# Kernel optimization log

Hardware: AMD Instinct MI355X
Metric: run time of the kernel (lower is better)

## Reference

```python
import jax, jax.numpy as jnp
import numpy as np

T, B, I, H, O = 512, 128, 512, 1024, 256

def setup_inputs() -> dict:
    key = jax.random.key(0)
    ks = jax.random.split(key, 7)
    s = 1.0 / np.sqrt(H)
    return {
        "seqs": jax.random.normal(ks[0], (T, B, I), dtype=jnp.float32),
        "W_ih": jax.random.uniform(ks[1], (H, I), minval=-s, maxval=s, dtype=jnp.float32),
        "W_hh": jax.random.uniform(ks[2], (H, H), minval=-s, maxval=s, dtype=jnp.float32),
        "b_ih": jax.random.uniform(ks[3], (H,), minval=-s, maxval=s, dtype=jnp.float32),
        "b_hh": jax.random.uniform(ks[4], (H,), minval=-s, maxval=s, dtype=jnp.float32),
        "W_fc": jax.random.uniform(ks[5], (O, H), minval=-s, maxval=s, dtype=jnp.float32),
        "b_fc": jax.random.uniform(ks[6], (O,), minval=-s, maxval=s, dtype=jnp.float32),
    }

def reference(seqs, W_ih, W_hh, b_ih, b_hh, W_fc, b_fc):
    # Precompute input projections for all timesteps in one big GEMM: [T,B,H]
    x_proj = jnp.einsum('tbi,hi->tbh', seqs, W_ih) + b_ih + b_hh

    def step(h, xp):
        h_new = jax.nn.relu(xp + h @ W_hh.T)
        return h_new, None

    h0 = jnp.zeros((seqs.shape[1], W_hh.shape[0]), dtype=seqs.dtype)
    h_final, _ = jax.lax.scan(step, h0, x_proj)
    return h_final @ W_fc.T + b_fc
```

## Files before the change

### kernel.cpp

```cpp
#include <hip/hip_runtime.h>
#include <hip/hip_bf16.h>
#include <stdint.h>

#define T_STEPS 512
#define BATCH   128
#define IN      512
#define HID     1024
#define OUTN    256

typedef __bf16 bf16x8 __attribute__((ext_vector_type(8)));
typedef float  f32x4  __attribute__((ext_vector_type(4)));
typedef unsigned short us8 __attribute__((ext_vector_type(8)));
typedef unsigned int   ui4 __attribute__((ext_vector_type(4)));

__device__ __forceinline__ unsigned short f2bf(float f) {
    uint32_t u = __float_as_uint(f);
    uint32_t r = (u + 0x7fffu + ((u >> 16) & 1u)) >> 16;
    return (unsigned short)r;
}

__device__ __forceinline__ ui4 ld_u128_agent(const void* p) {
    ui4 v;
    asm volatile("global_load_dwordx4 %0, %1, off sc0 sc1"
                 : "=v"(v) : "v"(p) : "memory");
    return v;
}

__device__ __forceinline__ bf16x8 ld_frag(const unsigned short* smem, int row, int kbyte, int rowstride) {
    int off = row * rowstride + (kbyte ^ ((row & 7) << 4));
    return *reinterpret_cast<const bf16x8*>(reinterpret_cast<const char*>(smem) + off);
}

__global__ __launch_bounds__(256, 1) void rnn_persistent(
    const float* __restrict__ seqs, const float* __restrict__ W_ih,
    const float* __restrict__ W_hh, const float* __restrict__ b_ih,
    const float* __restrict__ b_hh, const float* __restrict__ W_fc,
    const float* __restrict__ b_fc, float* __restrict__ out,
    unsigned short* __restrict__ hbuf,
    float* __restrict__ hfinal,
    unsigned int* __restrict__ flags)
{
    const int tid  = threadIdx.x;
    const int lane = tid & 63;
    const int wv   = tid >> 6;
    const int wg   = blockIdx.x;
    const int g    = wg >> 5;
    const int w    = wg & 31;
    const int gr0  = g * 16;
    const int c0   = w * 32;
    const int ln15 = lane & 15;
    const int lk   = lane >> 4;

    __shared__ unsigned short xtile[16 * 512];
    __shared__ unsigned short htile[16 * 1024];
    __shared__ float red[4][16][33];
    __shared__ float biasS[32];

    bf16x8 wih[2][4];
    bf16x8 whh[2][8];
    #pragma unroll
    for (int nt = 0; nt < 2; nt++) {
        const int j = c0 + nt * 16 + ln15;
        #pragma unroll
        for (int s = 0; s < 4; s++) {
            const int k = wv * 128 + s * 32 + lk * 8;
            const float* p = W_ih + j * IN + k;
            us8 u;
            #pragma unroll
            for (int e = 0; e < 8; e++) u[e] = f2bf(p[e]);
            wih[nt][s] = __builtin_bit_cast(bf16x8, u);
        }
        #pragma unroll
        for (int s = 0; s < 8; s++) {
            const int k = wv * 256 + s * 32 + lk * 8;
            const float* p = W_hh + j * HID + k;
            us8 u;
            #pragma unroll
            for (int e = 0; e < 8; e++) u[e] = f2bf(p[e]);
            whh[nt][s] = __builtin_bit_cast(bf16x8, u);
        }
    }
    if (tid < 32) biasS[tid] = b_ih[c0 + tid] + b_hh[c0 + tid];

    unsigned int* grp_flags = flags + g * 32;
    unsigned int* my_flag   = grp_flags + w;

    const int xrow[4] = { (tid) >> 6, (tid + 256) >> 6, (tid + 512) >> 6, (tid + 768) >> 6 };
    const int xcol[4] = { (tid) & 63, (tid + 256) & 63, (tid + 512) & 63, (tid + 768) & 63 };

    us8 xbf[4];
    {
        const float* xsrc = seqs + (size_t)gr0 * IN;
        #pragma unroll
        for (int it = 0; it < 4; it++) {
            const float* s4 = xsrc + xrow[it] * IN + xcol[it] * 8;
            float4 a = *reinterpret_cast<const float4*>(s4);
            float4 b = *reinterpret_cast<const float4*>(s4 + 4);
            us8 u;
            u[0]=f2bf(a.x); u[1]=f2bf(a.y); u[2]=f2bf(a.z); u[3]=f2bf(a.w);
            u[4]=f2bf(b.x); u[5]=f2bf(b.y); u[6]=f2bf(b.z); u[7]=f2bf(b.w);
            xbf[it] = u;
        }
    }

    for (int t = 0; t < T_STEPS; t++) {
        #pragma unroll
        for (int it = 0; it < 4; it++) {
            const int off = xrow[it] * 1024 + ((xcol[it] * 16) ^ ((xrow[it] & 7) << 4));
            *reinterpret_cast<us8*>(reinterpret_cast<char*>(xtile) + off) = xbf[it];
        }

        if (t > 0 && wv == 0 && lane < 32) {
            const unsigned int* f = grp_flags + lane;
            while (__hip_atomic_load(f, __ATOMIC_RELAXED, __HIP_MEMORY_SCOPE_AGENT) < (unsigned)t) {
                __builtin_amdgcn_s_sleep(1);
            }
        }
        __syncthreads();

        ui4 hv[8];
        if (t > 0) {
            const char* hsrc = reinterpret_cast<const char*>(
                hbuf + (size_t)(t & 1) * (BATCH * HID) + (size_t)gr0 * HID);
            #pragma unroll
            for (int it = 0; it < 8; it++) {
                const int c    = tid + it * 256;
                const int row  = c >> 7;
                const int colc = c & 127;
                hv[it] = ld_u128_agent(hsrc + row * 2048 + colc * 16);
            }
        }

        float4 xr[8];
        {
            const int tn = (t + 1 < T_STEPS) ? t + 1 : t;
            const float* xsrc = seqs + (size_t)tn * (BATCH * IN) + (size_t)gr0 * IN;
            #pragma unroll
            for (int it = 0; it < 4; it++) {
                const float* s4 = xsrc + xrow[it] * IN + xcol[it] * 8;
                xr[2*it]   = *reinterpret_cast<const float4*>(s4);
                xr[2*it+1] = *reinterpret_cast<const float4*>(s4 + 4);
            }
        }

        f32x4 acc0 = {0.f, 0.f, 0.f, 0.f};
        f32x4 acc1 = {0.f, 0.f, 0.f, 0.f};
        {
            const int kx0b = wv * 256;
            #pragma unroll
            for (int s = 0; s < 4; s++) {
                bf16x8 a = ld_frag(xtile, ln15, kx0b + s * 64 + lk * 16, 1024);
                acc0 = __builtin_amdgcn_mfma_f32_16x16x32_bf16(a, wih[0][s], acc0, 0, 0, 0);
                acc1 = __builtin_amdgcn_mfma_f32_16x16x32_bf16(a, wih[1][s], acc1, 0, 0, 0);
            }
        }

        if (t > 0) {
            asm volatile("s_waitcnt vmcnt(8)" ::: "memory");
            __builtin_amdgcn_sched_barrier(0);
            #pragma unroll
            for (int it = 0; it < 8; it++) {
                const int c    = tid + it * 256;
                const int row  = c >> 7;
                const int colc = c & 127;
                const int off = row * 2048 + ((colc * 16) ^ ((row & 7) << 4));
                *reinterpret_cast<ui4*>(reinterpret_cast<char*>(htile) + off) = hv[it];
            }
            __syncthreads();

            const int kh0b = wv * 512;
            #pragma unroll
            for (int s = 0; s < 8; s++) {
                bf16x8 a = ld_frag(htile, ln15, kh0b + s * 64 + lk * 16, 2048);
                acc0 = __builtin_amdgcn_mfma_f32_16x16x32_bf16(a, whh[0][s], acc0, 0, 0, 0);
                acc1 = __builtin_amdgcn_mfma_f32_16x16x32_bf16(a, whh[1][s], acc1, 0, 0, 0);
            }
        }

        #pragma unroll
        for (int r = 0; r < 4; r++) {
            red[wv][lk * 4 + r][ln15]      = acc0[r];
            red[wv][lk * 4 + r][16 + ln15] = acc1[r];
        }
        __syncthreads();
        {
            const int row = tid >> 4;
            const int co2 = (tid & 15) * 2;
            float v0 = red[0][row][co2]   + red[1][row][co2]   + red[2][row][co2]   + red[3][row][co2]   + biasS[co2];
            float v1 = red[0][row][co2+1] + red[1][row][co2+1] + red[2][row][co2+1] + red[3][row][co2+1] + biasS[co2+1];
            v0 = fmaxf(v0, 0.0f);
            v1 = fmaxf(v1, 0.0f);

            asm volatile("s_waitcnt vmcnt(0)" ::: "memory");
            __builtin_amdgcn_sched_barrier(0);
            #pragma unroll
            for (int it = 0; it < 4; it++) {
                float4 a = xr[2*it], b = xr[2*it+1];
                us8 u;
                u[0]=f2bf(a.x); u[1]=f2bf(a.y); u[2]=f2bf(a.z); u[3]=f2bf(a.w);
                u[4]=f2bf(b.x); u[5]=f2bf(b.y); u[6]=f2bf(b.z); u[7]=f2bf(b.w);
                xbf[it] = u;
            }

            if (t < T_STEPS - 1) {
                unsigned pack = (unsigned)f2bf(v0) | ((unsigned)f2bf(v1) << 16);
                unsigned* dst = reinterpret_cast<unsigned*>(
                    hbuf + (size_t)((t + 1) & 1) * (BATCH * HID) + (size_t)(gr0 + row) * HID + c0 + co2);
                __hip_atomic_store(dst, pack, __ATOMIC_RELAXED, __HIP_MEMORY_SCOPE_AGENT);
            } else {
                unsigned long long pack = ((unsigned long long)__float_as_uint(v1) << 32) | __float_as_uint(v0);
                unsigned long long* dst = reinterpret_cast<unsigned long long*>(
                    hfinal + (size_t)(gr0 + row) * HID + c0 + co2);
                __hip_atomic_store(dst, pack, __ATOMIC_RELAXED, __HIP_MEMORY_SCOPE_AGENT);
            }
        }
        asm volatile("s_waitcnt vmcnt(0)" ::: "memory");
        __syncthreads();
        if (tid == 0) {
            __hip_atomic_store(my_flag, (unsigned)(t + 1), __ATOMIC_RELAXED, __HIP_MEMORY_SCOPE_AGENT);
        }
    }

    if (wv == 0 && lane < 32) {
        const unsigned int* f = grp_flags + lane;
        while (__hip_atomic_load(f, __ATOMIC_RELAXED, __HIP_MEMORY_SCOPE_AGENT) < (unsigned)T_STEPS) {
            __builtin_amdgcn_s_sleep(1);
        }
    }
    __syncthreads();
    __threadfence();

    {
        const int oi   = tid & 127;
        const int half = tid >> 7;
        const int brow = gr0 + (oi >> 3);
        const int o    = w * 8 + (oi & 7);
        const float* hv2 = hfinal + (size_t)brow * HID + half * 512;
        const float* wf  = W_fc  + (size_t)o * HID + half * 512;
        float sum = 0.f;
        #pragma unroll 4
        for (int k = 0; k < 512; k += 4) {
            float4 hh = *reinterpret_cast<const float4*>(hv2 + k);
            float4 ww = *reinterpret_cast<const float4*>(wf + k);
            sum += hh.x * ww.x + hh.y * ww.y + hh.z * ww.z + hh.w * ww.w;
        }
        float* redf = &red[0][0][0];
        redf[tid] = sum;
        __syncthreads();
        if (tid < 128) {
            out[(size_t)brow * OUTN + o] = redf[tid] + redf[tid + 128] + b_fc[o];
        }
    }
}

extern "C" void kernel_launch(void* const* d_in, const int* in_sizes, int n_in,
                              void* d_out, int out_size, void* d_ws, size_t ws_size,
                              hipStream_t stream) {
    const float* seqs = (const float*)d_in[0];
    const float* W_ih = (const float*)d_in[1];
    const float* W_hh = (const float*)d_in[2];
    const float* b_ih = (const float*)d_in[3];
    const float* b_hh = (const float*)d_in[4];
    const float* W_fc = (const float*)d_in[5];
    const float* b_fc = (const float*)d_in[6];
    float* out = (float*)d_out;

    char* ws = (char*)d_ws;
    unsigned short* hbuf   = (unsigned short*)ws;
    float*          hfinal = (float*)(ws + 524288);
    unsigned int*   flags  = (unsigned int*)(ws + 1048576);

    hipMemsetAsync(flags, 0, 1024, stream);
    rnn_persistent<<<dim3(256), dim3(256), 0, stream>>>(
        seqs, W_ih, W_hh, b_ih, b_hh, W_fc, b_fc, out, hbuf, hfinal, flags);
}
```

Measured before the change: 1.396 ms.

## Replace per-step flag barrier with parity-tagged hidden-state data polling

```diff
diff --git a/kernel.cpp b/kernel.cpp
--- a/kernel.cpp
+++ b/kernel.cpp
@@ -13,6 +13,9 @@
 typedef unsigned short us8 __attribute__((ext_vector_type(8)));
 typedef unsigned int   ui4 __attribute__((ext_vector_type(4)));
 
+#define TAGM 0x80008000u
+#define CLRM 0x7FFF7FFFu
+
 __device__ __forceinline__ unsigned short f2bf(float f) {
     uint32_t u = __float_as_uint(f);
     uint32_t r = (u + 0x7fffu + ((u >> 16) & 1u)) >> 16;
@@ -30,15 +33,17 @@
     int off = row * rowstride + (kbyte ^ ((row & 7) << 4));
     return *reinterpret_cast<const bf16x8*>(reinterpret_cast<const char*>(smem) + off);
 }
+__device__ __forceinline__ us8 ld_frag_u(const unsigned short* smem, int row, int kbyte, int rowstride) {
+    int off = row * rowstride + (kbyte ^ ((row & 7) << 4));
+    return *reinterpret_cast<const us8*>(reinterpret_cast<const char*>(smem) + off);
+}
 
 __global__ __launch_bounds__(256, 1) void rnn_persistent(
     const float* __restrict__ seqs, const float* __restrict__ W_ih,
     const float* __restrict__ W_hh, const float* __restrict__ b_ih,
     const float* __restrict__ b_hh, const float* __restrict__ W_fc,
     const float* __restrict__ b_fc, float* __restrict__ out,
-    unsigned short* __restrict__ hbuf,
-    float* __restrict__ hfinal,
-    unsigned int* __restrict__ flags)
+    unsigned short* __restrict__ hbuf)
 {
     const int tid  = threadIdx.x;
     const int lane = tid & 63;
@@ -82,8 +87,15 @@
     }
     if (tid < 32) biasS[tid] = b_ih[c0 + tid] + b_hh[c0 + tid];
 
-    unsigned int* grp_flags = flags + g * 32;
-    unsigned int* my_flag   = grp_flags + w;
+    int hgoff[8], hloff[8];
+    #pragma unroll
+    for (int it = 0; it < 8; it++) {
+        const int c    = tid + it * 256;
+        const int row  = c >> 7;
+        const int colc = c & 127;
+        hgoff[it] = row * 2048 + colc * 16;
+        hloff[it] = row * 2048 + ((colc * 16) ^ ((row & 7) << 4));
+    }
 
     const int xrow[4] = { (tid) >> 6, (tid + 256) >> 6, (tid + 512) >> 6, (tid + 768) >> 6 };
     const int xcol[4] = { (tid) & 63, (tid + 256) & 63, (tid + 512) & 63, (tid + 768) & 63 };
@@ -103,33 +115,24 @@
         }
     }
 
+    const size_t slotB = (size_t)BATCH * HID * 2;
+    char* hbase = reinterpret_cast<char*>(hbuf);
+
     for (int t = 0; t < T_STEPS; t++) {
         #pragma unroll
         for (int it = 0; it < 4; it++) {
             const int off = xrow[it] * 1024 + ((xcol[it] * 16) ^ ((xrow[it] & 7) << 4));
             *reinterpret_cast<us8*>(reinterpret_cast<char*>(xtile) + off) = xbf[it];
         }
-
-        if (t > 0 && wv == 0 && lane < 32) {
-            const unsigned int* f = grp_flags + lane;
-            while (__hip_atomic_load(f, __ATOMIC_RELAXED, __HIP_MEMORY_SCOPE_AGENT) < (unsigned)t) {
-                __builtin_amdgcn_s_sleep(1);
-            }
-        }
         __syncthreads();
 
         ui4 hv[8];
+        const char* hsrc = hbase + (size_t)(t & 1) * slotB + (size_t)gr0 * HID * 2;
         if (t > 0) {
-            const char* hsrc = reinterpret_cast<const char*>(
-                hbuf + (size_t)(t & 1) * (BATCH * HID) + (size_t)gr0 * HID);
-            #pragma unroll
-            for (int it = 0; it < 8; it++) {
-                const int c    = tid + it * 256;
-                const int row  = c >> 7;
-                const int colc = c & 127;
-                hv[it] = ld_u128_agent(hsrc + row * 2048 + colc * 16);
-            }
-        }
+            #pragma unroll
+            for (int it = 0; it < 8; it++) hv[it] = ld_u128_agent(hsrc + hgoff[it]);
+        }
+        __builtin_amdgcn_sched_barrier(0);
 
         float4 xr[8];
         {
@@ -142,6 +145,7 @@
                 xr[2*it+1] = *reinterpret_cast<const float4*>(s4 + 4);
             }
         }
+        __builtin_amdgcn_sched_barrier(0);
 
         f32x4 acc0 = {0.f, 0.f, 0.f, 0.f};
         f32x4 acc1 = {0.f, 0.f, 0.f, 0.f};
@@ -156,15 +160,33 @@
         }
 
         if (t > 0) {
+            const unsigned pr = ((t >> 1) & 1) ? 0x80000000u : 0x00008000u;
             asm volatile("s_waitcnt vmcnt(8)" ::: "memory");
             __builtin_amdgcn_sched_barrier(0);
+            unsigned pending = 0xFFu;
+            while (true) {
+                unsigned np = 0;
+                #pragma unroll
+                for (int it = 0; it < 8; it++) {
+                    if (pending & (1u << it)) {
+                        unsigned d = ((hv[it][0] & TAGM) ^ pr) | ((hv[it][1] & TAGM) ^ pr)
+                                   | ((hv[it][2] & TAGM) ^ pr) | ((hv[it][3] & TAGM) ^ pr);
+                        if (d != 0u) {
+                            np |= (1u << it);
+                            hv[it] = ld_u128_agent(hsrc + hgoff[it]);
+                        }
+                    }
+                }
+                pending = np;
+                if (pending == 0u) break;
+                asm volatile("s_waitcnt vmcnt(0)" ::: "memory");
+                __builtin_amdgcn_sched_barrier(0);
+            }
             #pragma unroll
             for (int it = 0; it < 8; it++) {
-                const int c    = tid + it * 256;
-                const int row  = c >> 7;
-                const int colc = c & 127;
-                const int off = row * 2048 + ((colc * 16) ^ ((row & 7) << 4));
-                *reinterpret_cast<ui4*>(reinterpret_cast<char*>(htile) + off) = hv[it];
+                ui4 v = hv[it];
+                v[0] &= CLRM; v[1] &= CLRM; v[2] &= CLRM; v[3] &= CLRM;
+                *reinterpret_cast<ui4*>(reinterpret_cast<char*>(htile) + hloff[it]) = v;
             }
             __syncthreads();
 
@@ -183,72 +205,92 @@
             red[wv][lk * 4 + r][16 + ln15] = acc1[r];
         }
         __syncthreads();
+        const int hrow = tid >> 4;
+        const int co2  = (tid & 15) * 2;
+        float v0 = red[0][hrow][co2]   + red[1][hrow][co2]   + red[2][hrow][co2]   + red[3][hrow][co2]   + biasS[co2];
+        float v1 = red[0][hrow][co2+1] + red[1][hrow][co2+1] + red[2][hrow][co2+1] + red[3][hrow][co2+1] + biasS[co2+1];
+        v0 = fmaxf(v0, 0.0f);
+        v1 = fmaxf(v1, 0.0f);
+
+        asm volatile("s_waitcnt vmcnt(0)" ::: "memory");
+        __builtin_amdgcn_sched_barrier(0);
+        #pragma unroll
+        for (int it = 0; it < 4; it++) {
+            float4 a = xr[2*it], b = xr[2*it+1];
+            us8 u;
+            u[0]=f2bf(a.x); u[1]=f2bf(a.y); u[2]=f2bf(a.z); u[3]=f2bf(a.w);
+            u[4]=f2bf(b.x); u[5]=f2bf(b.y); u[6]=f2bf(b.z); u[7]=f2bf(b.w);
+            xbf[it] = u;
+        }
+
         {
-            const int row = tid >> 4;
-            const int co2 = (tid & 15) * 2;
-            float v0 = red[0][row][co2]   + red[1][row][co2]   + red[2][row][co2]   + red[3][row][co2]   + biasS[co2];
-            float v1 = red[0][row][co2+1] + red[1][row][co2+1] + red[2][row][co2+1] + red[3][row][co2+1] + biasS[co2+1];
-            v0 = fmaxf(v0, 0.0f);
-            v1 = fmaxf(v1, 0.0f);
-
+            const unsigned pw = (((t + 1) >> 1) & 1) ? 0x80000000u : 0x00008000u;
+            unsigned pack = (unsigned)f2bf(v0) | ((unsigned)f2bf(v1) << 16) | pw;
+            unsigned* dst = reinterpret_cast<unsigned*>(
+                hbase + (size_t)((t + 1) & 1) * slotB
+                + ((size_t)(gr0 + hrow) * HID + c0 + co2) * 2);
+            __hip_atomic_store(dst, pack, __ATOMIC_RELAXED, __HIP_MEMORY_SCOPE_AGENT);
+        }
+    }
+
+    {
+        const char* hsrc = hbase + (size_t)gr0 * HID * 2;
+        ui4 hv[8];
+        #pragma unroll
+        for (int it = 0; it < 8; it++) hv[it] = ld_u128_agent(hsrc + hgoff[it]);
+        unsigned pending = 0xFFu;
+        do {
             asm volatile("s_waitcnt vmcnt(0)" ::: "memory");
             __builtin_amdgcn_sched_barrier(0);
-            #pragma unroll
-            for (int it = 0; it < 4; it++) {
-                float4 a = xr[2*it], b = xr[2*it+1];
-                us8 u;
-                u[0]=f2bf(a.x); u[1]=f2bf(a.y); u[2]=f2bf(a.z); u[3]=f2bf(a.w);
-                u[4]=f2bf(b.x); u[5]=f2bf(b.y); u[6]=f2bf(b.z); u[7]=f2bf(b.w);
-                xbf[it] = u;
-            }
-
-            if (t < T_STEPS - 1) {
-                unsigned pack = (unsigned)f2bf(v0) | ((unsigned)f2bf(v1) << 16);
-                unsigned* dst = reinterpret_cast<unsigned*>(
-                    hbuf + (size_t)((t + 1) & 1) * (BATCH * HID) + (size_t)(gr0 + row) * HID + c0 + co2);
-                __hip_atomic_store(dst, pack, __ATOMIC_RELAXED, __HIP_MEMORY_SCOPE_AGENT);
-            } else {
-                unsigned long long pack = ((unsigned long long)__float_as_uint(v1) << 32) | __float_as_uint(v0);
-                unsigned long long* dst = reinterpret_cast<unsigned long long*>(
-                    hfinal + (size_t)(gr0 + row) * HID + c0 + co2);
-                __hip_atomic_store(dst, pack, __ATOMIC_RELAXED, __HIP_MEMORY_SCOPE_AGENT);
-            }
-        }
-        asm volatile("s_waitcnt vmcnt(0)" ::: "memory");
+            unsigned np = 0;
+            #pragma unroll
+            for (int it = 0; it < 8; it++) {
+                if (pending & (1u << it)) {
+                    unsigned d = ((hv[it][0] & TAGM) ^ 0x00008000u) | ((hv[it][1] & TAGM) ^ 0x00008000u)
+                               | ((hv[it][2] & TAGM) ^ 0x00008000u) | ((hv[it][3] & TAGM) ^ 0x00008000u);
+                    if (d != 0u) {
+                        np |= (1u << it);
+                        hv[it] = ld_u128_agent(hsrc + hgoff[it]);
+                    }
+                }
+            }
+            pending = np;
+        } while (pending);
+        #pragma unroll
+        for (int it = 0; it < 8; it++) {
+            ui4 v = hv[it];
+            v[0] &= CLRM; v[1] &= CLRM; v[2] &= CLRM; v[3] &= CLRM;
+            *reinterpret_cast<ui4*>(reinterpret_cast<char*>(htile) + hloff[it]) = v;
+        }
         __syncthreads();
-        if (tid == 0) {
-            __hip_atomic_store(my_flag, (unsigned)(t + 1), __ATOMIC_RELAXED, __HIP_MEMORY_SCOPE_AGENT);
-        }
-    }
-
-    if (wv == 0 && lane < 32) {
-        const unsigned int* f = grp_flags + lane;
-        while (__hip_atomic_load(f, __ATOMIC_RELAXED, __HIP_MEMORY_SCOPE_AGENT) < (unsigned)T_STEPS) {
-            __builtin_amdgcn_s_sleep(1);
-        }
-    }
-    __syncthreads();
-    __threadfence();
+    }
 
     {
         const int oi   = tid & 127;
         const int half = tid >> 7;
-        const int brow = gr0 + (oi >> 3);
+        const int row  = oi >> 3;
         const int o    = w * 8 + (oi & 7);
-        const float* hv2 = hfinal + (size_t)brow * HID + half * 512;
-        const float* wf  = W_fc  + (size_t)o * HID + half * 512;
+        const float* wf = W_fc + (size_t)o * HID + half * 512;
         float sum = 0.f;
         #pragma unroll 4
-        for (int k = 0; k < 512; k += 4) {
-            float4 hh = *reinterpret_cast<const float4*>(hv2 + k);
-            float4 ww = *reinterpret_cast<const float4*>(wf + k);
-            sum += hh.x * ww.x + hh.y * ww.y + hh.z * ww.z + hh.w * ww.w;
+        for (int ck = 0; ck < 64; ck++) {
+            us8 hu = ld_frag_u(htile, row, half * 1024 + ck * 16, 2048);
+            float4 wa = *reinterpret_cast<const float4*>(wf + ck * 8);
+            float4 wb = *reinterpret_cast<const float4*>(wf + ck * 8 + 4);
+            sum += __uint_as_float((unsigned)hu[0] << 16) * wa.x
+                 + __uint_as_float((unsigned)hu[1] << 16) * wa.y
+                 + __uint_as_float((unsigned)hu[2] << 16) * wa.z
+                 + __uint_as_float((unsigned)hu[3] << 16) * wa.w
+                 + __uint_as_float((unsigned)hu[4] << 16) * wb.x
+                 + __uint_as_float((unsigned)hu[5] << 16) * wb.y
+                 + __uint_as_float((unsigned)hu[6] << 16) * wb.z
+                 + __uint_as_float((unsigned)hu[7] << 16) * wb.w;
         }
         float* redf = &red[0][0][0];
         redf[tid] = sum;
         __syncthreads();
         if (tid < 128) {
-            out[(size_t)brow * OUTN + o] = redf[tid] + redf[tid + 128] + b_fc[o];
+            out[(size_t)(gr0 + row) * OUTN + o] = redf[tid] + redf[tid + 128] + b_fc[o];
         }
     }
 }
@@ -265,12 +307,9 @@
     const float* b_fc = (const float*)d_in[6];
     float* out = (float*)d_out;
 
-    char* ws = (char*)d_ws;
-    unsigned short* hbuf   = (unsigned short*)ws;
-    float*          hfinal = (float*)(ws + 524288);
-    unsigned int*   flags  = (unsigned int*)(ws + 1048576);
-
-    hipMemsetAsync(flags, 0, 1024, stream);
+    unsigned short* hbuf = (unsigned short*)d_ws;
+
+    hipMemsetAsync(hbuf, 0, 2 * BATCH * HID * sizeof(unsigned short), stream);
     rnn_persistent<<<dim3(256), dim3(256), 0, stream>>>(
-        seqs, W_ih, W_hh, b_ih, b_hh, W_fc, b_fc, out, hbuf, hfinal, flags);
-}
+        seqs, W_ih, W_hh, b_ih, b_hh, W_fc, b_fc, out, hbuf);
+}
```

Result: slower. 1.594 ms (+14.2%).

## Load recurrent h fragments straight into MFMA registers and pad flags

Applied to the files above, without the earlier changes.

```diff
diff --git a/kernel.cpp b/kernel.cpp
--- a/kernel.cpp
+++ b/kernel.cpp
@@ -52,7 +52,6 @@
     const int lk   = lane >> 4;
 
     __shared__ unsigned short xtile[16 * 512];
-    __shared__ unsigned short htile[16 * 1024];
     __shared__ float red[4][16][33];
     __shared__ float biasS[32];
 
@@ -82,8 +81,10 @@
     }
     if (tid < 32) biasS[tid] = b_ih[c0 + tid] + b_hh[c0 + tid];
 
-    unsigned int* grp_flags = flags + g * 32;
-    unsigned int* my_flag   = grp_flags + w;
+    unsigned int* grp_flags = flags + g * 32 * 16;
+    unsigned int* my_flag   = grp_flags + w * 16;
+
+    const int hfrag = ln15 * 2048 + wv * 512 + lk * 16;
 
     const int xrow[4] = { (tid) >> 6, (tid + 256) >> 6, (tid + 512) >> 6, (tid + 768) >> 6 };
     const int xcol[4] = { (tid) & 63, (tid + 256) & 63, (tid + 512) & 63, (tid + 768) & 63 };
@@ -103,32 +104,14 @@
         }
     }
 
+    const size_t slotB = (size_t)BATCH * HID * 2;
+    char* hbase = reinterpret_cast<char*>(hbuf);
+
     for (int t = 0; t < T_STEPS; t++) {
         #pragma unroll
         for (int it = 0; it < 4; it++) {
             const int off = xrow[it] * 1024 + ((xcol[it] * 16) ^ ((xrow[it] & 7) << 4));
             *reinterpret_cast<us8*>(reinterpret_cast<char*>(xtile) + off) = xbf[it];
-        }
-
-        if (t > 0 && wv == 0 && lane < 32) {
-            const unsigned int* f = grp_flags + lane;
-            while (__hip_atomic_load(f, __ATOMIC_RELAXED, __HIP_MEMORY_SCOPE_AGENT) < (unsigned)t) {
-                __builtin_amdgcn_s_sleep(1);
-            }
-        }
-        __syncthreads();
-
-        ui4 hv[8];
-        if (t > 0) {
-            const char* hsrc = reinterpret_cast<const char*>(
-                hbuf + (size_t)(t & 1) * (BATCH * HID) + (size_t)gr0 * HID);
-            #pragma unroll
-            for (int it = 0; it < 8; it++) {
-                const int c    = tid + it * 256;
-                const int row  = c >> 7;
-                const int colc = c & 127;
-                hv[it] = ld_u128_agent(hsrc + row * 2048 + colc * 16);
-            }
         }
 
         float4 xr[8];
@@ -143,6 +126,22 @@
             }
         }
 
+        if (t > 0 && wv == 0 && lane < 32) {
+            const unsigned int* f = grp_flags + lane * 16;
+            while (__hip_atomic_load(f, __ATOMIC_RELAXED, __HIP_MEMORY_SCOPE_AGENT) < (unsigned)t) {
+                __builtin_amdgcn_s_sleep(1);
+            }
+        }
+        __syncthreads();
+
+        ui4 hv[8];
+        if (t > 0) {
+            const char* hsrc = hbase + (size_t)(t & 1) * slotB + (size_t)gr0 * 2048 + hfrag;
+            #pragma unroll
+            for (int s = 0; s < 8; s++) hv[s] = ld_u128_agent(hsrc + s * 64);
+        }
+        __builtin_amdgcn_sched_barrier(0);
+
         f32x4 acc0 = {0.f, 0.f, 0.f, 0.f};
         f32x4 acc1 = {0.f, 0.f, 0.f, 0.f};
         {
@@ -156,22 +155,11 @@
         }
 
         if (t > 0) {
-            asm volatile("s_waitcnt vmcnt(8)" ::: "memory");
+            asm volatile("s_waitcnt vmcnt(0)" ::: "memory");
             __builtin_amdgcn_sched_barrier(0);
             #pragma unroll
-            for (int it = 0; it < 8; it++) {
-                const int c    = tid + it * 256;
-                const int row  = c >> 7;
-                const int colc = c & 127;
-                const int off = row * 2048 + ((colc * 16) ^ ((row & 7) << 4));
-                *reinterpret_cast<ui4*>(reinterpret_cast<char*>(htile) + off) = hv[it];
-            }
-            __syncthreads();
-
-            const int kh0b = wv * 512;
-            #pragma unroll
             for (int s = 0; s < 8; s++) {
-                bf16x8 a = ld_frag(htile, ln15, kh0b + s * 64 + lk * 16, 2048);
+                bf16x8 a = __builtin_bit_cast(bf16x8, hv[s]);
                 acc0 = __builtin_amdgcn_mfma_f32_16x16x32_bf16(a, whh[0][s], acc0, 0, 0, 0);
                 acc1 = __builtin_amdgcn_mfma_f32_16x16x32_bf16(a, whh[1][s], acc1, 0, 0, 0);
             }
@@ -183,46 +171,46 @@
             red[wv][lk * 4 + r][16 + ln15] = acc1[r];
         }
         __syncthreads();
-        {
-            const int row = tid >> 4;
-            const int co2 = (tid & 15) * 2;
-            float v0 = red[0][row][co2]   + red[1][row][co2]   + red[2][row][co2]   + red[3][row][co2]   + biasS[co2];
-            float v1 = red[0][row][co2+1] + red[1][row][co2+1] + red[2][row][co2+1] + red[3][row][co2+1] + biasS[co2+1];
-            v0 = fmaxf(v0, 0.0f);
-            v1 = fmaxf(v1, 0.0f);
-
-            asm volatile("s_waitcnt vmcnt(0)" ::: "memory");
-            __builtin_amdgcn_sched_barrier(0);
-            #pragma unroll
-            for (int it = 0; it < 4; it++) {
-                float4 a = xr[2*it], b = xr[2*it+1];
-                us8 u;
-                u[0]=f2bf(a.x); u[1]=f2bf(a.y); u[2]=f2bf(a.z); u[3]=f2bf(a.w);
-                u[4]=f2bf(b.x); u[5]=f2bf(b.y); u[6]=f2bf(b.z); u[7]=f2bf(b.w);
-                xbf[it] = u;
-            }
-
-            if (t < T_STEPS - 1) {
-                unsigned pack = (unsigned)f2bf(v0) | ((unsigned)f2bf(v1) << 16);
-                unsigned* dst = reinterpret_cast<unsigned*>(
-                    hbuf + (size_t)((t + 1) & 1) * (BATCH * HID) + (size_t)(gr0 + row) * HID + c0 + co2);
-                __hip_atomic_store(dst, pack, __ATOMIC_RELAXED, __HIP_MEMORY_SCOPE_AGENT);
-            } else {
-                unsigned long long pack = ((unsigned long long)__float_as_uint(v1) << 32) | __float_as_uint(v0);
-                unsigned long long* dst = reinterpret_cast<unsigned long long*>(
-                    hfinal + (size_t)(gr0 + row) * HID + c0 + co2);
-                __hip_atomic_store(dst, pack, __ATOMIC_RELAXED, __HIP_MEMORY_SCOPE_AGENT);
-            }
-        }
+
+        const int hrow = tid >> 4;
+        const int co2  = (tid & 15) * 2;
+        float v0 = red[0][hrow][co2]   + red[1][hrow][co2]   + red[2][hrow][co2]   + red[3][hrow][co2]   + biasS[co2];
+        float v1 = red[0][hrow][co2+1] + red[1][hrow][co2+1] + red[2][hrow][co2+1] + red[3][hrow][co2+1] + biasS[co2+1];
+        v0 = fmaxf(v0, 0.0f);
+        v1 = fmaxf(v1, 0.0f);
+
+        if (t < T_STEPS - 1) {
+            unsigned pack = (unsigned)f2bf(v0) | ((unsigned)f2bf(v1) << 16);
+            unsigned* dst = reinterpret_cast<unsigned*>(
+                hbase + (size_t)((t + 1) & 1) * slotB
+                + ((size_t)(gr0 + hrow) * HID + c0 + co2) * 2);
+            __hip_atomic_store(dst, pack, __ATOMIC_RELAXED, __HIP_MEMORY_SCOPE_AGENT);
+        } else {
+            unsigned long long pack = ((unsigned long long)__float_as_uint(v1) << 32) | __float_as_uint(v0);
+            unsigned long long* dst = reinterpret_cast<unsigned long long*>(
+                hfinal + (size_t)(gr0 + hrow) * HID + c0 + co2);
+            __hip_atomic_store(dst, pack, __ATOMIC_RELAXED, __HIP_MEMORY_SCOPE_AGENT);
+        }
+
         asm volatile("s_waitcnt vmcnt(0)" ::: "memory");
+        __builtin_amdgcn_sched_barrier(0);
         __syncthreads();
         if (tid == 0) {
             __hip_atomic_store(my_flag, (unsigned)(t + 1), __ATOMIC_RELAXED, __HIP_MEMORY_SCOPE_AGENT);
         }
+
+        #pragma unroll
+        for (int it = 0; it < 4; it++) {
+            float4 a = xr[2*it], b = xr[2*it+1];
+            us8 u;
+            u[0]=f2bf(a.x); u[1]=f2bf(a.y); u[2]=f2bf(a.z); u[3]=f2bf(a.w);
+            u[4]=f2bf(b.x); u[5]=f2bf(b.y); u[6]=f2bf(b.z); u[7]=f2bf(b.w);
+            xbf[it] = u;
+        }
     }
 
     if (wv == 0 && lane < 32) {
-        const unsigned int* f = grp_flags + lane;
+        const unsigned int* f = grp_flags + lane * 16;
         while (__hip_atomic_load(f, __ATOMIC_RELAXED, __HIP_MEMORY_SCOPE_AGENT) < (unsigned)T_STEPS) {
             __builtin_amdgcn_s_sleep(1);
         }
@@ -270,7 +258,7 @@
     float*          hfinal = (float*)(ws + 524288);
     unsigned int*   flags  = (unsigned int*)(ws + 1048576);
 
-    hipMemsetAsync(flags, 0, 1024, stream);
+    hipMemsetAsync(flags, 0, 8 * 32 * 64, stream);
     rnn_persistent<<<dim3(256), dim3(256), 0, stream>>>(
         seqs, W_ih, W_hh, b_ih, b_hh, W_fc, b_fc, out, hbuf, hfinal, flags);
 }
```

After: 1.543 ms. 1.11x slower.
